# Performance work log

Hardware: AMD Instinct MI355X
Metric: run time of the kernel (lower is better)

The kernel has to match this reference:

```python
import jax, jax.numpy as jnp
import numpy as np

DEPTH = 24; D_MODEL = 192; D_INNER = 384; D_STATE = 16; DT_RANK = 12; D_CONV = 4
H = 32; W = 3200; P = 16; NP = (W // P) * (H // P)  # 400 patches
NCLS = 22; BATCH = 4; EPS = 1e-5


def _rmsnorm(x, w):
    return x * jax.lax.rsqrt(jnp.mean(x * x, axis=-1, keepdims=True) + EPS) * w


def _causal_dwconv(x, w, b):
    # x: (B, L, D), w: (D, K) depthwise, left-padded causal conv (mamba conv1d)
    D = x.shape[-1]; K = w.shape[-1]
    xp = jnp.pad(jnp.swapaxes(x, 1, 2), ((0, 0), (0, 0), (K - 1, 0)))
    y = jax.lax.conv_general_dilated(xp, w[:, None, :], (1,), 'VALID',
            dimension_numbers=('NCH', 'OIH', 'NCH'), feature_group_count=D)
    return jnp.swapaxes(y + b[None, :, None], 1, 2)


def _selective_scan(x, dt, Bm, Cm, A, Dsk):
    # x, dt: (B, L, d); Bm, Cm: (B, L, n); A: (d, n); Dsk: (d,)
    dA = jnp.exp(dt[..., None] * A)                  # (B, L, d, n)
    dBx = (dt * x)[..., None] * Bm[:, :, None, :]    # (B, L, d, n)
    h0 = jnp.zeros((x.shape[0], x.shape[2], A.shape[1]), x.dtype)

    def step(h, inp):
        a, bx, c = inp
        h = a * h + bx
        return h, jnp.einsum('bdn,bn->bd', h, c)

    _, ys = jax.lax.scan(step, h0,
        (jnp.swapaxes(dA, 0, 1), jnp.swapaxes(dBx, 0, 1), jnp.swapaxes(Cm, 0, 1)))
    return jnp.swapaxes(ys, 0, 1) + x * Dsk


def _mamba_dir(xz, cw_l, cb_l, xpw, dtw, dtb, A, Dsk):
    xx, z = jnp.split(xz, 2, axis=-1)
    xx = jax.nn.silu(_causal_dwconv(xx, cw_l, cb_l))
    dbl = xx @ xpw.T                                  # (B, L, dt_rank + 2n)
    dt = jax.nn.softplus(dbl[..., :DT_RANK] @ dtw.T + dtb)
    Bm = dbl[..., DT_RANK:DT_RANK + D_STATE]
    Cm = dbl[..., DT_RANK + D_STATE:]
    y = _selective_scan(xx, dt, Bm, Cm, A, Dsk)
    return y * jax.nn.silu(z)


def _forward(x, pe_w, pe_b, cls_token, pos_embed, norm_w, in_proj_w, cw, cb,
             xproj_w, dtproj_w, dtproj_b, A_log, A_b_log, Dp, outproj_w,
             norm_f_w, head_w, head_b):
    B = x.shape[0]
    # patch embed: conv2d stride=kernel=16 on (B,1,H,W)
    y = jax.lax.conv_general_dilated(x[:, None], pe_w, (P, P), 'VALID',
            dimension_numbers=('NCHW', 'OIHW', 'NCHW')) + pe_b[None, :, None, None]
    tok = jnp.transpose(y, (0, 2, 3, 1)).reshape(B, -1, D_MODEL)   # (B, NP, D)
    tok = jnp.concatenate([jnp.broadcast_to(cls_token, (B, 1, D_MODEL)), tok], axis=1)
    tok = tok + pos_embed

    def layer_step(carry, p):
        hidden, residual = carry
        nw, ipw, cw_l, cb_l, xpw, dtw, dtb, Al, Abl, Dsk, opw = p
        residual = residual + hidden          # fused add (residual_in_fp32: all fp32)
        h = _rmsnorm(residual, nw)
        xz = h @ ipw.T                         # (B, L, 2*d_inner)
        y_f = _mamba_dir(xz, cw_l, cb_l, xpw, dtw, dtb, -jnp.exp(Al), Dsk)
        y_b = _mamba_dir(xz[:, ::-1], cw_l, cb_l, xpw, dtw, dtb, -jnp.exp(Abl), Dsk)[:, ::-1]
        return ((y_f + y_b) @ opw.T, residual), None

    # NOTE: source sets residual = x AND hidden = x before the loop, so the
    (hidden, residual), _ = jax.lax.scan(
        layer_step, (tok, tok),
        (norm_w, in_proj_w, cw, cb, xproj_w, dtproj_w, dtproj_b, A_log, A_b_log, Dp, outproj_w))
    out = _rmsnorm(residual + hidden, norm_f_w)
    return out[:, 0] @ head_w.T + head_b          # (B, n_classes)


def setup_inputs() -> dict:
    key = jax.random.key(0)
    ks = jax.random.split(key, 12)

    def n(k, shape, scale):
        return jax.random.normal(k, shape, jnp.float32) * scale

    a_init = jnp.tile(jnp.log(jnp.arange(1, D_STATE + 1, dtype=jnp.float32))[None, None, :],
                      (DEPTH, D_INNER, 1))
    return {
        'x': n(ks[0], (BATCH, H, W), 1.0),
        'pe_w': n(ks[1], (D_MODEL, 1, P, P), 1.0 / P),
        'pe_b': jnp.zeros((D_MODEL,), jnp.float32),
        'cls_token': n(ks[2], (1, 1, D_MODEL), 0.02),
        'pos_embed': n(ks[3], (1, NP + 1, D_MODEL), 0.02),
        'norm_w': jnp.ones((DEPTH, D_MODEL), jnp.float32),
        'in_proj_w': n(ks[4], (DEPTH, 2 * D_INNER, D_MODEL), D_MODEL ** -0.5),
        'cw': n(ks[5], (DEPTH, D_INNER, D_CONV), D_CONV ** -0.5),
        'cb': jnp.zeros((DEPTH, D_INNER), jnp.float32),
        'xproj_w': n(ks[6], (DEPTH, DT_RANK + 2 * D_STATE, D_INNER), D_INNER ** -0.5),
        'dtproj_w': n(ks[7], (DEPTH, D_INNER, DT_RANK), DT_RANK ** -0.5),
        'dtproj_b': n(ks[8], (DEPTH, D_INNER), 0.1),
        'A_log': a_init,
        'A_b_log': a_init,
        'Dp': jnp.ones((DEPTH, D_INNER), jnp.float32),
        'outproj_w': n(ks[9], (DEPTH, D_MODEL, D_INNER), D_INNER ** -0.5 / np.sqrt(DEPTH)),
        'norm_f_w': jnp.ones((D_MODEL,), jnp.float32),
        'head_w': n(ks[10], (NCLS, D_MODEL), D_MODEL ** -0.5),
        'head_b': jnp.zeros((NCLS,), jnp.float32),
    }


def reference(x, pe_w, pe_b, cls_token, pos_embed, norm_w, in_proj_w, cw, cb,
              xproj_w, dtproj_w, dtproj_b, A_log, A_b_log, Dp, outproj_w,
              norm_f_w, head_w, head_b):
    return _forward(x, pe_w, pe_b, cls_token, pos_embed, norm_w, in_proj_w, cw, cb,
                    xproj_w, dtproj_w, dtproj_b, A_log, A_b_log, Dp, outproj_w,
                    norm_f_w, head_w, head_b)
```

## Files before the change

kernel.cpp:

```cpp
#include <hip/hip_runtime.h>
#include <hip/hip_bf16.h>

#define DEPTH 24
#define DM 192
#define DI 384
#define DS 16
#define DR 12
#define LSEQ 401
#define BATCH 4
#define NTOK (BATCH*LSEQ)
#define NCLS 22
#define NC 16
#define TCH 26

__device__ __forceinline__ float silu_f(float x) { return x / (1.f + __expf(-x)); }

__global__ void patch_embed_k(const float* __restrict__ x,
                              const float* __restrict__ pe_w,
                              const float* __restrict__ pe_b,
                              const float* __restrict__ cls,
                              const float* __restrict__ pos,
                              float* __restrict__ residual, float* __restrict__ hidden)
{
    __shared__ float xp[4][256];
    int g0 = blockIdx.x * 4;
    int c = threadIdx.x;
    #pragma unroll
    for (int j = 0; j < 4; j++) {
        int g = g0 + j;
        int b = g / LSEQ, t = g % LSEQ;
        if (t != 0) {
            int p = t - 1, pi = p / 200, pj = p % 200;
            for (int i = c; i < 256; i += 192) {
                int pp = i >> 4, qq = i & 15;
                xp[j][i] = x[((size_t)(b * 32 + pi * 16 + pp)) * 3200 + pj * 16 + qq];
            }
        }
    }
    __syncthreads();
    float acc[4] = {0.f, 0.f, 0.f, 0.f};
    for (int k = 0; k < 256; k++) {
        float w = pe_w[c * 256 + k];
        #pragma unroll
        for (int j = 0; j < 4; j++) acc[j] += xp[j][k] * w;
    }
    #pragma unroll
    for (int j = 0; j < 4; j++) {
        int g = g0 + j;
        int t = g % LSEQ;
        float v = (t == 0) ? cls[c] : (acc[j] + pe_b[c]);
        v += pos[t * DM + c];
        residual[(size_t)g * DM + c] = v;
        hidden[(size_t)g * DM + c] = v;
    }
}

__global__ __launch_bounds__(256) void gemm_xz_k(
    const float* __restrict__ resin, const float* __restrict__ hidden,
    float* __restrict__ resout, const float* __restrict__ nw,
    const float* __restrict__ ipw, float* __restrict__ xz,
    float* __restrict__ dbl)
{
    __shared__ float As[48][68];
    __shared__ float Ws[48][68];
    __shared__ float srms[64];
    __shared__ float ps[64][4];
    int tid = threadIdx.x;
    for (int i = (blockIdx.y * 12 + blockIdx.x) * 256 + tid; i < 2 * NTOK * 44; i += 312 * 256)
        dbl[i] = 0.f;
    int bn = blockIdx.x * 64;
    int bm = blockIdx.y * 64;
    int rr = tid >> 2, q = tid & 3;
    int m = bm + rr;
    float rv[4][12];
    float s = 0.f;
    if (m < NTOK) {
        const float* rp = resin + (size_t)m * DM;
        const float* hp = hidden + (size_t)m * DM;
        #pragma unroll
        for (int c = 0; c < 4; c++) {
            int base = c * 48 + q * 12;
            #pragma unroll
            for (int i = 0; i < 12; i += 4) {
                float4 a = *(const float4*)&rp[base + i];
                float4 b = *(const float4*)&hp[base + i];
                float r0 = a.x + b.x, r1 = a.y + b.y, r2 = a.z + b.z, r3 = a.w + b.w;
                rv[c][i] = r0; rv[c][i + 1] = r1; rv[c][i + 2] = r2; rv[c][i + 3] = r3;
                s += r0 * r0 + r1 * r1 + r2 * r2 + r3 * r3;
            }
        }
        if (bn == 0) {
            float* op = resout + (size_t)m * DM;
            #pragma unroll
            for (int c = 0; c < 4; c++) {
                int base = c * 48 + q * 12;
                #pragma unroll
                for (int i = 0; i < 12; i += 4)
                    *(float4*)&op[base + i] =
                        make_float4(rv[c][i], rv[c][i + 1], rv[c][i + 2], rv[c][i + 3]);
            }
        }
    } else {
        #pragma unroll
        for (int c = 0; c < 4; c++)
            #pragma unroll
            for (int i = 0; i < 12; i++) rv[c][i] = 0.f;
    }
    ps[rr][q] = s;
    __syncthreads();
    if (q == 0) {
        float tot = ps[rr][0] + ps[rr][1] + ps[rr][2] + ps[rr][3];
        srms[rr] = rsqrtf(tot * (1.f / (float)DM) + 1e-5f);
    }
    __syncthreads();

    int orow = (tid >> 4) * 4;
    int ocol = (tid & 15) * 4;
    int sk = q * 12;
    float acc[4][4] = {};
    for (int c = 0; c < 4; c++) {
        float rs = srms[rr];
        #pragma unroll
        for (int i = 0; i < 12; i++)
            As[sk + i][rr] = rv[c][i] * rs * nw[c * 48 + sk + i];
        const float* wp = ipw + (size_t)(bn + rr) * DM + c * 48 + sk;
        #pragma unroll
        for (int i = 0; i < 12; i++)
            Ws[sk + i][rr] = wp[i];
        __syncthreads();
        #pragma unroll
        for (int kk = 0; kk < 48; kk++) {
            float4 a = *(const float4*)&As[kk][orow];
            float4 w = *(const float4*)&Ws[kk][ocol];
            acc[0][0] += a.x * w.x; acc[0][1] += a.x * w.y; acc[0][2] += a.x * w.z; acc[0][3] += a.x * w.w;
            acc[1][0] += a.y * w.x; acc[1][1] += a.y * w.y; acc[1][2] += a.y * w.z; acc[1][3] += a.y * w.w;
            acc[2][0] += a.z * w.x; acc[2][1] += a.z * w.y; acc[2][2] += a.z * w.z; acc[2][3] += a.z * w.w;
            acc[3][0] += a.w * w.x; acc[3][1] += a.w * w.y; acc[3][2] += a.w * w.z; acc[3][3] += a.w * w.w;
        }
        __syncthreads();
    }
    #pragma unroll
    for (int i = 0; i < 4; i++) {
        int mm = bm + orow + i;
        if (mm >= NTOK) continue;
        *(float4*)&xz[(size_t)mm * (2 * DI) + bn + ocol] =
            make_float4(acc[i][0], acc[i][1], acc[i][2], acc[i][3]);
    }
}

__global__ __launch_bounds__(256) void xproj_conv_k(
    const float* __restrict__ xz,
    const float* __restrict__ cw, const float* __restrict__ cb,
    const float* __restrict__ xpw, float* __restrict__ dbl,
    float* __restrict__ hidden)
{
    __shared__ float As[96][33];
    __shared__ float Ws[96][48];
    int tid = threadIdx.x;
    for (int i = (blockIdx.y * 4 + blockIdx.x) * 256 + tid; i < NTOK * DM; i += 404 * 256)
        hidden[i] = 0.f;
    int kbase = blockIdx.x * 96;
    int bm = blockIdx.y * 32;
    for (int idx = tid; idx < 96 * 32; idx += 256) {
        int k = idx >> 5, row = idx & 31;
        int m = bm + row;
        float v = 0.f;
        if (m < 2 * NTOK) {
            int dir = m / NTOK;
            int r = m - dir * NTOK;
            int b = r / LSEQ, t = r % LSEQ;
            int ch = kbase + k;
            float a = cb[ch];
            #pragma unroll
            for (int j = 0; j < 4; j++) {
                int tt = t - 3 + j;
                if (tt >= 0) {
                    int st = dir ? (LSEQ - 1 - tt) : tt;
                    a += cw[ch * 4 + j] * xz[((size_t)(b * LSEQ + st)) * (2 * DI) + ch];
                }
            }
            v = silu_f(a);
        }
        As[k][row] = v;
    }
    for (int i = tid; i < 96 * 48; i += 256) {
        int k = i / 48, rr = i % 48;
        Ws[k][rr] = (rr < 44) ? xpw[(size_t)rr * DI + kbase + k] : 0.f;
    }
    __syncthreads();
    int row = tid & 31, cg = tid >> 5;
    int cbase = cg * 6;
    float acc[6] = {};
    #pragma unroll 4
    for (int kk = 0; kk < 96; kk++) {
        float a = As[kk][row];
        #pragma unroll
        for (int j = 0; j < 6; j++) acc[j] += a * Ws[kk][cbase + j];
    }
    int m = bm + row;
    if (m < 2 * NTOK) {
        #pragma unroll
        for (int j = 0; j < 6; j++) {
            int cc = cbase + j;
            if (cc < 44) atomicAdd(&dbl[(size_t)m * 44 + cc], acc[j]);
        }
    }
}

__global__ __launch_bounds__(256) void scan_part_k(
    const float* __restrict__ xz, const float* __restrict__ dbl,
    const float* __restrict__ cw, const float* __restrict__ cb,
    const float* __restrict__ dtw, const float* __restrict__ dtb,
    const float* __restrict__ A_log, const float* __restrict__ A_b_log,
    float* __restrict__ hloc, float* __restrict__ Pc)
{
    __shared__ float sdbl[TCH][28];
    __shared__ float sdt[TCH][16];
    __shared__ float sxx[TCH][16];
    __shared__ float sw[16][12];
    __shared__ float sb2[16];
    int dblk = blockIdx.x, chunk = blockIdx.y;
    int db = blockIdx.z;
    int dir = db >> 2, b = db & 3;
    int tid = threadIdx.x;
    int d0 = dblk * 16;
    int t0 = chunk * TCH;
    size_t dof44 = (size_t)db * LSEQ * 44;
    for (int i = tid; i < TCH * 28; i += 256) {
        int t = i / 28, cc = i - t * 28;
        sdbl[t][cc] = dbl[dof44 + (size_t)(t0 + t) * 44 + cc];
    }
    if (tid < 192) { int d = tid / 12, r = tid - d * 12; sw[d][r] = dtw[(size_t)(d0 + d) * 12 + r]; }
    if (tid < 16) sb2[tid] = dtb[d0 + tid];
    for (int i = tid; i < TCH * 16; i += 256) {
        int t = i >> 4, d = i & 15;
        int tq = t0 + t, ch = d0 + d;
        float a = cb[ch];
        #pragma unroll
        for (int j = 0; j < 4; j++) {
            int tt = tq - 3 + j;
            if (tt >= 0) {
                int st = dir ? (LSEQ - 1 - tt) : tt;
                a += cw[ch * 4 + j] * xz[((size_t)(b * LSEQ + st)) * (2 * DI) + ch];
            }
        }
        sxx[t][d] = silu_f(a);
    }
    __syncthreads();
    for (int i = tid; i < TCH * 16; i += 256) {
        int t = i >> 4, d = i & 15;
        float a2 = sb2[d];
        #pragma unroll
        for (int r = 0; r < 12; r++) a2 += sdbl[t][r] * sw[d][r];
        sdt[t][d] = (a2 > 15.f) ? a2 : __logf(1.f + __expf(a2));
    }
    __syncthreads();
    int wave = tid >> 6, lane = tid & 63;
    int dsub = wave * 4 + (lane >> 4);
    int n = lane & 15;
    const float* Al = dir ? A_b_log : A_log;
    float Aval = -__expf(Al[(d0 + dsub) * DS + n]);
    float h = 0.f, P = 1.f;
    #pragma unroll
    for (int i = 0; i < TCH; i++) {
        float dtv = sdt[i][dsub];
        float xv  = sxx[i][dsub];
        float Bv  = sdbl[i][12 + n];
        float dA = __expf(dtv * Aval);
        h = dA * h + (dtv * xv) * Bv;
        P *= dA;
    }
    size_t idx2 = ((size_t)db * NC + chunk) * (DI * DS) + (size_t)(d0 + dsub) * DS + n;
    hloc[idx2] = h;
    Pc[idx2] = P;
}

__global__ __launch_bounds__(256) void scan_fix_k(
    const float* __restrict__ xz, const float* __restrict__ dbl,
    const float* __restrict__ cw, const float* __restrict__ cb,
    const float* __restrict__ dtw, const float* __restrict__ dtb,
    const float* __restrict__ A_log, const float* __restrict__ A_b_log,
    const float* __restrict__ Dp,
    const float* __restrict__ hloc, const float* __restrict__ Pc,
    float* __restrict__ yraw)
{
    __shared__ float sdbl[TCH][44];
    __shared__ float sdt[TCH][16];
    __shared__ float sxx[TCH][16];
    __shared__ float sy[TCH][16];
    __shared__ float sw[16][12];
    __shared__ float sb2[16];
    int dblk = blockIdx.x, chunk = blockIdx.y;
    int db = blockIdx.z;
    int dir = db >> 2, b = db & 3;
    int tid = threadIdx.x;
    int d0 = dblk * 16;
    int t0 = chunk * TCH;
    size_t dofD = (size_t)db * LSEQ * DI;
    size_t dof44 = (size_t)db * LSEQ * 44;
    for (int i = tid; i < TCH * 44; i += 256) {
        int t = i / 44, cc = i - t * 44;
        sdbl[t][cc] = ((t0 + t) < LSEQ) ? dbl[dof44 + (size_t)(t0 + t) * 44 + cc] : 0.f;
    }
    if (tid < 192) { int d = tid / 12, r = tid - d * 12; sw[d][r] = dtw[(size_t)(d0 + d) * 12 + r]; }
    if (tid < 16) sb2[tid] = dtb[d0 + tid];
    for (int i = tid; i < TCH * 16; i += 256) {
        int t = i >> 4, d = i & 15;
        int tq = t0 + t, ch = d0 + d;
        float v = 0.f;
        if (tq < LSEQ) {
            float a = cb[ch];
            #pragma unroll
            for (int j = 0; j < 4; j++) {
                int tt = tq - 3 + j;
                if (tt >= 0) {
                    int st = dir ? (LSEQ - 1 - tt) : tt;
                    a += cw[ch * 4 + j] * xz[((size_t)(b * LSEQ + st)) * (2 * DI) + ch];
                }
            }
            v = silu_f(a);
        }
        sxx[t][d] = v;
    }
    __syncthreads();
    for (int i = tid; i < TCH * 16; i += 256) {
        int t = i >> 4, d = i & 15;
        float a2 = sb2[d];
        #pragma unroll
        for (int r = 0; r < 12; r++) a2 += sdbl[t][r] * sw[d][r];
        sdt[t][d] = (a2 > 15.f) ? a2 : __logf(1.f + __expf(a2));
    }
    __syncthreads();
    int wave = tid >> 6, lane = tid & 63;
    int dsub = wave * 4 + (lane >> 4);
    int n = lane & 15;
    const float* Al = dir ? A_b_log : A_log;
    float Aval = -__expf(Al[(d0 + dsub) * DS + n]);
    float Dv = Dp[d0 + dsub];
    float h = 0.f;
    size_t cbase = (size_t)db * NC * (DI * DS) + (size_t)(d0 + dsub) * DS + n;
    #pragma unroll
    for (int j = 0; j < NC - 1; j++) {
        size_t idx = cbase + (size_t)j * (DI * DS);
        float pj = Pc[idx], hj = hloc[idx];
        h = (j < chunk) ? (pj * h + hj) : h;
    }
    #pragma unroll
    for (int i = 0; i < TCH; i++) {
        float dtv = sdt[i][dsub];
        float xv  = sxx[i][dsub];
        float Bv  = sdbl[i][12 + n];
        float Cv  = sdbl[i][28 + n];
        h = __expf(dtv * Aval) * h + (dtv * xv) * Bv;
        float p = h * Cv;
        p += __shfl_xor(p, 1);
        p += __shfl_xor(p, 2);
        p += __shfl_xor(p, 4);
        p += __shfl_xor(p, 8);
        if (n == 0) sy[i][dsub] = p + xv * Dv;
    }
    __syncthreads();
    int len = min(t0 + TCH, LSEQ) - t0;
    for (int idx = tid; idx < len * 16; idx += 256) {
        int t = idx >> 4, d = idx & 15;
        yraw[dofD + (size_t)(t0 + t) * DI + d0 + d] = sy[t][d];
    }
}

__global__ __launch_bounds__(256) void outproj_k(
    const float* __restrict__ yraw, const float* __restrict__ xz,
    const float* __restrict__ opw, float* __restrict__ hidden)
{
    __shared__ float As[96][34];
    __shared__ float Ws[96][34];
    int tid = threadIdx.x;
    int bn = blockIdx.x * 32;
    int bm = blockIdx.y * 32;
    int kbase = blockIdx.z * 192;
    int row8 = tid >> 3, seg = tid & 7, k0 = seg * 24;
    float a[24], wreg[24];
    int m = bm + row8;
    if (m < NTOK) {
        int b = m / LSEQ, t = m % LSEQ;
        const float* yf = yraw + (size_t)m * DI + kbase + k0;
        const float* yb = yraw + (size_t)(NTOK + b * LSEQ + (LSEQ - 1 - t)) * DI + kbase + k0;
        const float* zp = xz + (size_t)m * (2 * DI) + DI + kbase + k0;
        #pragma unroll
        for (int i = 0; i < 24; i++) {
            float z = zp[i];
            a[i] = (yf[i] + yb[i]) * (z / (1.f + __expf(-z)));
        }
    } else {
        #pragma unroll
        for (int i = 0; i < 24; i++) a[i] = 0.f;
    }
    {
        const float* wp = opw + (size_t)(bn + row8) * DI + kbase + k0;
        #pragma unroll
        for (int i = 0; i < 24; i++) wreg[i] = wp[i];
    }
    int r0 = (tid >> 4) * 2, c0 = (tid & 15) * 2;
    float acc[2][2] = {};
    #pragma unroll
    for (int st = 0; st < 2; st++) {
        if (st) __syncthreads();
        if ((seg >> 2) == st) {
            int kb = k0 - st * 96;
            #pragma unroll
            for (int i = 0; i < 24; i++) {
                As[kb + i][row8] = a[i];
                Ws[kb + i][row8] = wreg[i];
            }
        }
        __syncthreads();
        #pragma unroll 8
        for (int kk = 0; kk < 96; kk++) {
            float2 av = *(const float2*)&As[kk][r0];
            float2 wv = *(const float2*)&Ws[kk][c0];
            acc[0][0] += av.x * wv.x; acc[0][1] += av.x * wv.y;
            acc[1][0] += av.y * wv.x; acc[1][1] += av.y * wv.y;
        }
    }
    #pragma unroll
    for (int i = 0; i < 2; i++) {
        int mm = bm + r0 + i;
        if (mm >= NTOK) continue;
        #pragma unroll
        for (int j = 0; j < 2; j++)
            atomicAdd(&hidden[(size_t)mm * DM + bn + c0 + j], acc[i][j]);
    }
}

__global__ void final_head_k(const float* __restrict__ residual, const float* __restrict__ hidden,
                             const float* __restrict__ norm_f,
                             const float* __restrict__ head_w,
                             const float* __restrict__ head_b,
                             void* __restrict__ out,
                             const unsigned short* __restrict__ probe)
{
    __shared__ float wsum[3];
    __shared__ float hb[DM];
    int b = blockIdx.x;
    int c = threadIdx.x;
    int idx = (b * LSEQ) * DM + c;
    float r = residual[idx] + hidden[idx];
    float s = r * r;
    for (int off = 32; off > 0; off >>= 1) s += __shfl_down(s, off);
    int wave = c >> 6, lane = c & 63;
    if (lane == 0) wsum[wave] = s;
    __syncthreads();
    float tot = wsum[0] + wsum[1] + wsum[2];
    float rms = rsqrtf(tot / (float)DM + 1e-5f);
    hb[c] = r * rms * norm_f[c];
    __syncthreads();
    if (c < NCLS) {
        float acc = head_b[c];
        #pragma unroll 8
        for (int k = 0; k < DM; k++) acc += hb[k] * head_w[c * DM + k];
        if (probe[0] == 0x3F80u)
            ((__hip_bfloat16*)out)[b * NCLS + c] = __float2bfloat16(acc);
        else
            ((float*)out)[b * NCLS + c] = acc;
    }
}

extern "C" void kernel_launch(void* const* d_in, const int* in_sizes, int n_in,
                              void* d_out, int out_size, void* d_ws, size_t ws_size,
                              hipStream_t stream)
{
    (void)in_sizes; (void)n_in; (void)out_size; (void)ws_size;
    const float* x      = (const float*)d_in[0];
    const float* pe_w   = (const float*)d_in[1];
    const float* pe_b   = (const float*)d_in[2];
    const float* cls    = (const float*)d_in[3];
    const float* pos    = (const float*)d_in[4];
    const float* norm_w = (const float*)d_in[5];
    const float* ipw    = (const float*)d_in[6];
    const float* cw     = (const float*)d_in[7];
    const float* cb     = (const float*)d_in[8];
    const float* xpw    = (const float*)d_in[9];
    const float* dtw    = (const float*)d_in[10];
    const float* dtb    = (const float*)d_in[11];
    const float* A_log  = (const float*)d_in[12];
    const float* A_b_log= (const float*)d_in[13];
    const float* Dp     = (const float*)d_in[14];
    const float* opw    = (const float*)d_in[15];
    const float* norm_f = (const float*)d_in[16];
    const float* head_w = (const float*)d_in[17];
    const float* head_b = (const float*)d_in[18];
    const unsigned short* probe = (const unsigned short*)d_in[14];

    float* ws = (float*)d_ws;
    const size_t nTokDM = (size_t)NTOK * DM;
    const size_t nTokXZ = (size_t)NTOK * 2 * DI;
    const size_t nDirDI = (size_t)2 * NTOK * DI;
    const size_t nDir44 = (size_t)2 * NTOK * 44;
    const size_t nChunk = (size_t)2 * BATCH * NC * DI * DS;
    float* resA   = ws;
    float* resB   = resA + nTokDM;
    float* hidden = resB + nTokDM;
    float* xz     = hidden + nTokDM;
    float* dbl    = xz + nTokXZ;
    float* yraw   = dbl + nDir44;
    float* hloc   = yraw + nDirDI;
    float* Pc     = hloc + nChunk;

    patch_embed_k<<<NTOK / 4, DM, 0, stream>>>(x, pe_w, pe_b, cls, pos, resA, hidden);

    for (int l = 0; l < DEPTH; l++) {
        float* rin  = (l & 1) ? resB : resA;
        float* rout = (l & 1) ? resA : resB;

        gemm_xz_k<<<dim3(12, 26), 256, 0, stream>>>(
            rin, hidden, rout, norm_w + (size_t)l * DM,
            ipw + (size_t)l * 2 * DI * DM, xz, dbl);

        xproj_conv_k<<<dim3(4, 101), 256, 0, stream>>>(
            xz, cw + (size_t)l * DI * 4, cb + (size_t)l * DI,
            xpw + (size_t)l * 44 * DI, dbl, hidden);

        scan_part_k<<<dim3(DI / 16, NC - 1, 2 * BATCH), 256, 0, stream>>>(
            xz, dbl, cw + (size_t)l * DI * 4, cb + (size_t)l * DI,
            dtw + (size_t)l * DI * DR, dtb + (size_t)l * DI,
            A_log + (size_t)l * DI * DS, A_b_log + (size_t)l * DI * DS,
            hloc, Pc);

        scan_fix_k<<<dim3(DI / 16, NC, 2 * BATCH), 256, 0, stream>>>(
            xz, dbl, cw + (size_t)l * DI * 4, cb + (size_t)l * DI,
            dtw + (size_t)l * DI * DR, dtb + (size_t)l * DI,
            A_log + (size_t)l * DI * DS, A_b_log + (size_t)l * DI * DS,
            Dp + (size_t)l * DI, hloc, Pc, yraw);

        outproj_k<<<dim3(6, 51, 2), 256, 0, stream>>>(
            yraw, xz, opw + (size_t)l * DM * DI, hidden);
    }

    final_head_k<<<BATCH, DM, 0, stream>>>(resA, hidden, norm_f, head_w, head_b,
                                           d_out, probe);
}
```

Measured before the change: 3.156 ms.

## Map one channel per thread with all 16 states in registers in scan kernels

Both chunked scan kernels change from 16 lanes per channel (one state each) to one thread per channel holding all 16 states in registers, with a 384-thread block covering every channel of a chunk. The conv, dt projection and softplus are computed per thread in registers with a sliding window, so the shared-memory staging, extra barriers and the shuffle reduction for C·h go away. This also coalesces the hloc/Pc layout across channels. In exchange the grid shrinks from thousands of blocks to 120/128 blocks, which leaves most CUs idle and adds register pressure from the large per-thread arrays.

```diff
diff --git a/kernel.cpp b/kernel.cpp
--- a/kernel.cpp
+++ b/kernel.cpp
@@ -207,7 +207,7 @@
     }
 }
 
-__global__ __launch_bounds__(256) void scan_part_k(
+__global__ __launch_bounds__(384) void scan_part_k(
     const float* __restrict__ xz, const float* __restrict__ dbl,
     const float* __restrict__ cw, const float* __restrict__ cb,
     const float* __restrict__ dtw, const float* __restrict__ dtb,
@@ -215,67 +215,83 @@
     float* __restrict__ hloc, float* __restrict__ Pc)
 {
     __shared__ float sdbl[TCH][28];
-    __shared__ float sdt[TCH][16];
-    __shared__ float sxx[TCH][16];
-    __shared__ float sw[16][12];
-    __shared__ float sb2[16];
-    int dblk = blockIdx.x, chunk = blockIdx.y;
-    int db = blockIdx.z;
+    int chunk = blockIdx.x, db = blockIdx.y;
     int dir = db >> 2, b = db & 3;
     int tid = threadIdx.x;
-    int d0 = dblk * 16;
     int t0 = chunk * TCH;
     size_t dof44 = (size_t)db * LSEQ * 44;
-    for (int i = tid; i < TCH * 28; i += 256) {
+    for (int i = tid; i < TCH * 28; i += 384) {
         int t = i / 28, cc = i - t * 28;
         sdbl[t][cc] = dbl[dof44 + (size_t)(t0 + t) * 44 + cc];
     }
-    if (tid < 192) { int d = tid / 12, r = tid - d * 12; sw[d][r] = dtw[(size_t)(d0 + d) * 12 + r]; }
-    if (tid < 16) sb2[tid] = dtb[d0 + tid];
-    for (int i = tid; i < TCH * 16; i += 256) {
-        int t = i >> 4, d = i & 15;
-        int tq = t0 + t, ch = d0 + d;
-        float a = cb[ch];
-        #pragma unroll
-        for (int j = 0; j < 4; j++) {
-            int tt = tq - 3 + j;
-            if (tt >= 0) {
-                int st = dir ? (LSEQ - 1 - tt) : tt;
-                a += cw[ch * 4 + j] * xz[((size_t)(b * LSEQ + st)) * (2 * DI) + ch];
-            }
-        }
-        sxx[t][d] = silu_f(a);
-    }
-    __syncthreads();
-    for (int i = tid; i < TCH * 16; i += 256) {
-        int t = i >> 4, d = i & 15;
-        float a2 = sb2[d];
-        #pragma unroll
-        for (int r = 0; r < 12; r++) a2 += sdbl[t][r] * sw[d][r];
-        sdt[t][d] = (a2 > 15.f) ? a2 : __logf(1.f + __expf(a2));
-    }
-    __syncthreads();
-    int wave = tid >> 6, lane = tid & 63;
-    int dsub = wave * 4 + (lane >> 4);
-    int n = lane & 15;
-    const float* Al = dir ? A_b_log : A_log;
-    float Aval = -__expf(Al[(d0 + dsub) * DS + n]);
-    float h = 0.f, P = 1.f;
-    #pragma unroll
-    for (int i = 0; i < TCH; i++) {
-        float dtv = sdt[i][dsub];
-        float xv  = sxx[i][dsub];
-        float Bv  = sdbl[i][12 + n];
-        float dA = __expf(dtv * Aval);
-        h = dA * h + (dtv * xv) * Bv;
-        P *= dA;
-    }
-    size_t idx2 = ((size_t)db * NC + chunk) * (DI * DS) + (size_t)(d0 + dsub) * DS + n;
-    hloc[idx2] = h;
-    Pc[idx2] = P;
-}
-
-__global__ __launch_bounds__(256) void scan_fix_k(
+    __syncthreads();
+    int d = tid;
+    float cw0 = cw[d * 4], cw1 = cw[d * 4 + 1], cw2 = cw[d * 4 + 2], cw3 = cw[d * 4 + 3];
+    float cbv = cb[d];
+    float dtwv[12];
+    #pragma unroll
+    for (int r = 0; r < 12; r += 4) {
+        float4 v = *(const float4*)&dtw[(size_t)d * 12 + r];
+        dtwv[r] = v.x; dtwv[r + 1] = v.y; dtwv[r + 2] = v.z; dtwv[r + 3] = v.w;
+    }
+    float dtbv = dtb[d];
+    const float* xcol = xz + d;
+    float w0, w1, w2, w3;
+    {
+        int tt;
+        tt = t0 - 3; w0 = (tt >= 0) ? xcol[(size_t)(b * LSEQ + (dir ? LSEQ - 1 - tt : tt)) * (2 * DI)] : 0.f;
+        tt = t0 - 2; w1 = (tt >= 0) ? xcol[(size_t)(b * LSEQ + (dir ? LSEQ - 1 - tt : tt)) * (2 * DI)] : 0.f;
+        tt = t0 - 1; w2 = (tt >= 0) ? xcol[(size_t)(b * LSEQ + (dir ? LSEQ - 1 - tt : tt)) * (2 * DI)] : 0.f;
+    }
+    float xxv[TCH], dtv[TCH];
+    #pragma unroll
+    for (int t = 0; t < TCH; t++) {
+        int tt = t0 + t;
+        w3 = xcol[(size_t)(b * LSEQ + (dir ? LSEQ - 1 - tt : tt)) * (2 * DI)];
+        float a = cbv + cw0 * w0 + cw1 * w1 + cw2 * w2 + cw3 * w3;
+        w0 = w1; w1 = w2; w2 = w3;
+        xxv[t] = silu_f(a);
+        float a2 = dtbv;
+        #pragma unroll
+        for (int r = 0; r < 12; r++) a2 += sdbl[t][r] * dtwv[r];
+        dtv[t] = (a2 > 15.f) ? a2 : __logf(1.f + __expf(a2));
+    }
+    const float* Al = (dir ? A_b_log : A_log) + (size_t)d * DS;
+    float Aval[16];
+    #pragma unroll
+    for (int n = 0; n < 16; n += 4) {
+        float4 v = *(const float4*)&Al[n];
+        Aval[n] = -__expf(v.x); Aval[n + 1] = -__expf(v.y);
+        Aval[n + 2] = -__expf(v.z); Aval[n + 3] = -__expf(v.w);
+    }
+    float h[16], P[16];
+    #pragma unroll
+    for (int n = 0; n < 16; n++) { h[n] = 0.f; P[n] = 1.f; }
+    #pragma unroll
+    for (int t = 0; t < TCH; t++) {
+        float u = dtv[t] * xxv[t];
+        #pragma unroll
+        for (int n4 = 0; n4 < 16; n4 += 4) {
+            float4 Bv = *(const float4*)&sdbl[t][12 + n4];
+            float dA0 = __expf(dtv[t] * Aval[n4 + 0]);
+            float dA1 = __expf(dtv[t] * Aval[n4 + 1]);
+            float dA2 = __expf(dtv[t] * Aval[n4 + 2]);
+            float dA3 = __expf(dtv[t] * Aval[n4 + 3]);
+            h[n4 + 0] = dA0 * h[n4 + 0] + u * Bv.x; P[n4 + 0] *= dA0;
+            h[n4 + 1] = dA1 * h[n4 + 1] + u * Bv.y; P[n4 + 1] *= dA1;
+            h[n4 + 2] = dA2 * h[n4 + 2] + u * Bv.z; P[n4 + 2] *= dA2;
+            h[n4 + 3] = dA3 * h[n4 + 3] + u * Bv.w; P[n4 + 3] *= dA3;
+        }
+    }
+    size_t base = (size_t)(db * NC + chunk) * DS * DI + d;
+    #pragma unroll
+    for (int n = 0; n < 16; n++) {
+        hloc[base + (size_t)n * DI] = h[n];
+        Pc[base + (size_t)n * DI] = P[n];
+    }
+}
+
+__global__ __launch_bounds__(384) void scan_fix_k(
     const float* __restrict__ xz, const float* __restrict__ dbl,
     const float* __restrict__ cw, const float* __restrict__ cb,
     const float* __restrict__ dtw, const float* __restrict__ dtb,
@@ -285,85 +301,93 @@
     float* __restrict__ yraw)
 {
     __shared__ float sdbl[TCH][44];
-    __shared__ float sdt[TCH][16];
-    __shared__ float sxx[TCH][16];
-    __shared__ float sy[TCH][16];
-    __shared__ float sw[16][12];
-    __shared__ float sb2[16];
-    int dblk = blockIdx.x, chunk = blockIdx.y;
-    int db = blockIdx.z;
+    int chunk = blockIdx.x, db = blockIdx.y;
     int dir = db >> 2, b = db & 3;
     int tid = threadIdx.x;
-    int d0 = dblk * 16;
     int t0 = chunk * TCH;
+    int len = min(LSEQ - t0, TCH);
+    size_t dof44 = (size_t)db * LSEQ * 44;
     size_t dofD = (size_t)db * LSEQ * DI;
-    size_t dof44 = (size_t)db * LSEQ * 44;
-    for (int i = tid; i < TCH * 44; i += 256) {
+    for (int i = tid; i < len * 44; i += 384) {
         int t = i / 44, cc = i - t * 44;
-        sdbl[t][cc] = ((t0 + t) < LSEQ) ? dbl[dof44 + (size_t)(t0 + t) * 44 + cc] : 0.f;
-    }
-    if (tid < 192) { int d = tid / 12, r = tid - d * 12; sw[d][r] = dtw[(size_t)(d0 + d) * 12 + r]; }
-    if (tid < 16) sb2[tid] = dtb[d0 + tid];
-    for (int i = tid; i < TCH * 16; i += 256) {
-        int t = i >> 4, d = i & 15;
-        int tq = t0 + t, ch = d0 + d;
-        float v = 0.f;
-        if (tq < LSEQ) {
-            float a = cb[ch];
-            #pragma unroll
-            for (int j = 0; j < 4; j++) {
-                int tt = tq - 3 + j;
-                if (tt >= 0) {
-                    int st = dir ? (LSEQ - 1 - tt) : tt;
-                    a += cw[ch * 4 + j] * xz[((size_t)(b * LSEQ + st)) * (2 * DI) + ch];
-                }
+        sdbl[t][cc] = dbl[dof44 + (size_t)(t0 + t) * 44 + cc];
+    }
+    __syncthreads();
+    int d = tid;
+    float cw0 = cw[d * 4], cw1 = cw[d * 4 + 1], cw2 = cw[d * 4 + 2], cw3 = cw[d * 4 + 3];
+    float cbv = cb[d];
+    float dtwv[12];
+    #pragma unroll
+    for (int r = 0; r < 12; r += 4) {
+        float4 v = *(const float4*)&dtw[(size_t)d * 12 + r];
+        dtwv[r] = v.x; dtwv[r + 1] = v.y; dtwv[r + 2] = v.z; dtwv[r + 3] = v.w;
+    }
+    float dtbv = dtb[d];
+    const float* xcol = xz + d;
+    float w0, w1, w2, w3;
+    {
+        int tt;
+        tt = t0 - 3; w0 = (tt >= 0) ? xcol[(size_t)(b * LSEQ + (dir ? LSEQ - 1 - tt : tt)) * (2 * DI)] : 0.f;
+        tt = t0 - 2; w1 = (tt >= 0) ? xcol[(size_t)(b * LSEQ + (dir ? LSEQ - 1 - tt : tt)) * (2 * DI)] : 0.f;
+        tt = t0 - 1; w2 = (tt >= 0) ? xcol[(size_t)(b * LSEQ + (dir ? LSEQ - 1 - tt : tt)) * (2 * DI)] : 0.f;
+    }
+    float xxv[TCH], dtv[TCH];
+    #pragma unroll
+    for (int t = 0; t < TCH; t++) {
+        if (t < len) {
+            int tt = t0 + t;
+            w3 = xcol[(size_t)(b * LSEQ + (dir ? LSEQ - 1 - tt : tt)) * (2 * DI)];
+            float a = cbv + cw0 * w0 + cw1 * w1 + cw2 * w2 + cw3 * w3;
+            w0 = w1; w1 = w2; w2 = w3;
+            xxv[t] = silu_f(a);
+            float a2 = dtbv;
+            #pragma unroll
+            for (int r = 0; r < 12; r++) a2 += sdbl[t][r] * dtwv[r];
+            dtv[t] = (a2 > 15.f) ? a2 : __logf(1.f + __expf(a2));
+        } else { xxv[t] = 0.f; dtv[t] = 0.f; }
+    }
+    const float* Al = (dir ? A_b_log : A_log) + (size_t)d * DS;
+    float Aval[16];
+    #pragma unroll
+    for (int n = 0; n < 16; n += 4) {
+        float4 v = *(const float4*)&Al[n];
+        Aval[n] = -__expf(v.x); Aval[n + 1] = -__expf(v.y);
+        Aval[n + 2] = -__expf(v.z); Aval[n + 3] = -__expf(v.w);
+    }
+    float Dv = Dp[d];
+    float h[16];
+    #pragma unroll
+    for (int n = 0; n < 16; n++) h[n] = 0.f;
+    size_t cb2 = (size_t)(db * NC) * DS * DI + d;
+    for (int j = 0; j < chunk; j++) {
+        size_t bj = cb2 + (size_t)j * DS * DI;
+        #pragma unroll
+        for (int n = 0; n < 16; n++) {
+            float pj = Pc[bj + (size_t)n * DI];
+            float hj = hloc[bj + (size_t)n * DI];
+            h[n] = pj * h[n] + hj;
+        }
+    }
+    #pragma unroll
+    for (int t = 0; t < TCH; t++) {
+        if (t < len) {
+            float u = dtv[t] * xxv[t];
+            float p = 0.f;
+            #pragma unroll
+            for (int n4 = 0; n4 < 16; n4 += 4) {
+                float4 Bv = *(const float4*)&sdbl[t][12 + n4];
+                float4 Cv = *(const float4*)&sdbl[t][28 + n4];
+                float dA0 = __expf(dtv[t] * Aval[n4 + 0]);
+                float dA1 = __expf(dtv[t] * Aval[n4 + 1]);
+                float dA2 = __expf(dtv[t] * Aval[n4 + 2]);
+                float dA3 = __expf(dtv[t] * Aval[n4 + 3]);
+                h[n4 + 0] = dA0 * h[n4 + 0] + u * Bv.x; p += h[n4 + 0] * Cv.x;
+                h[n4 + 1] = dA1 * h[n4 + 1] + u * Bv.y; p += h[n4 + 1] * Cv.y;
+                h[n4 + 2] = dA2 * h[n4 + 2] + u * Bv.z; p += h[n4 + 2] * Cv.z;
+                h[n4 + 3] = dA3 * h[n4 + 3] + u * Bv.w; p += h[n4 + 3] * Cv.w;
             }
-            v = silu_f(a);
-        }
-        sxx[t][d] = v;
-    }
-    __syncthreads();
-    for (int i = tid; i < TCH * 16; i += 256) {
-        int t = i >> 4, d = i & 15;
-        float a2 = sb2[d];
-        #pragma unroll
-        for (int r = 0; r < 12; r++) a2 += sdbl[t][r] * sw[d][r];
-        sdt[t][d] = (a2 > 15.f) ? a2 : __logf(1.f + __expf(a2));
-    }
-    __syncthreads();
-    int wave = tid >> 6, lane = tid & 63;
-    int dsub = wave * 4 + (lane >> 4);
-    int n = lane & 15;
-    const float* Al = dir ? A_b_log : A_log;
-    float Aval = -__expf(Al[(d0 + dsub) * DS + n]);
-    float Dv = Dp[d0 + dsub];
-    float h = 0.f;
-    size_t cbase = (size_t)db * NC * (DI * DS) + (size_t)(d0 + dsub) * DS + n;
-    #pragma unroll
-    for (int j = 0; j < NC - 1; j++) {
-        size_t idx = cbase + (size_t)j * (DI * DS);
-        float pj = Pc[idx], hj = hloc[idx];
-        h = (j < chunk) ? (pj * h + hj) : h;
-    }
-    #pragma unroll
-    for (int i = 0; i < TCH; i++) {
-        float dtv = sdt[i][dsub];
-        float xv  = sxx[i][dsub];
-        float Bv  = sdbl[i][12 + n];
-        float Cv  = sdbl[i][28 + n];
-        h = __expf(dtv * Aval) * h + (dtv * xv) * Bv;
-        float p = h * Cv;
-        p += __shfl_xor(p, 1);
-        p += __shfl_xor(p, 2);
-        p += __shfl_xor(p, 4);
-        p += __shfl_xor(p, 8);
-        if (n == 0) sy[i][dsub] = p + xv * Dv;
-    }
-    __syncthreads();
-    int len = min(t0 + TCH, LSEQ) - t0;
-    for (int idx = tid; idx < len * 16; idx += 256) {
-        int t = idx >> 4, d = idx & 15;
-        yraw[dofD + (size_t)(t0 + t) * DI + d0 + d] = sy[t][d];
+            yraw[dofD + (size_t)(t0 + t) * DI + d] = p + xxv[t] * Dv;
+        }
     }
 }
 
@@ -519,13 +543,13 @@
             xz, cw + (size_t)l * DI * 4, cb + (size_t)l * DI,
             xpw + (size_t)l * 44 * DI, dbl, hidden);
 
-        scan_part_k<<<dim3(DI / 16, NC - 1, 2 * BATCH), 256, 0, stream>>>(
+        scan_part_k<<<dim3(NC - 1, 2 * BATCH), 384, 0, stream>>>(
             xz, dbl, cw + (size_t)l * DI * 4, cb + (size_t)l * DI,
             dtw + (size_t)l * DI * DR, dtb + (size_t)l * DI,
             A_log + (size_t)l * DI * DS, A_b_log + (size_t)l * DI * DS,
             hloc, Pc);
 
-        scan_fix_k<<<dim3(DI / 16, NC, 2 * BATCH), 256, 0, stream>>>(
+        scan_fix_k<<<dim3(NC, 2 * BATCH), 384, 0, stream>>>(
             xz, dbl, cw + (size_t)l * DI * 4, cb + (size_t)l * DI,
             dtw + (size_t)l * DI * DR, dtb + (size_t)l * DI,
             A_log + (size_t)l * DI * DS, A_b_log + (size_t)l * DI * DS,
```

Result: slower. 3.488 ms (+10.5%).
